# Performance work log

Hardware: AMD Instinct MI355X
Metric: run time of the kernel (lower is better)

## Reference

```python
import jax, jax.numpy as jnp
import numpy as np

EPS = 1e-8
N_NODES, N_EDGES = 10000, 160000
SI, VI = 128, 16          # node scalar / vector channels
ES, EV = 32, 4            # edge scalar / vector channels
SO, VO = 128, 16          # output scalar / vector channels
MSI, MVI = 2 * SI + ES, 2 * VI + EV   # message input dims: 288, 36
H1 = max(MVI, VO)         # layer-1 hidden = 36 (bottleneck=1)
H2 = max(VO, VO)          # layer-2 hidden = 16
SVO = 3                   # scalarization_vectorization_output_dim


def _safe_norm(x, axis):
    return jnp.sqrt(jnp.sum(x * x, axis=axis) + EPS)


def _gcp(s, v, frames, Wdown, Wdf, Wso, bso, Wup, Wg, bg):
    """GCP block on edge-level inputs (node_inputs=False, vector_gate=True).
    s: [E, si], v: [E, vi, 3], frames: [E, 3, 3]."""
    v_pre = jnp.swapaxes(v, -1, -2)                 # [E, 3, vi]
    v_hid = v_pre @ Wdown                           # [E, 3, h]
    v_norm = _safe_norm(v_hid, axis=-2)             # [E, h]
    v_frames = v_pre @ Wdf                          # [E, 3, svo]
    # scalarize: frames @ v_frames -> [E,3,svo], transpose -> [E,svo,3], flatten to 9
    local = jnp.swapaxes(frames @ v_frames, -1, -2).reshape(v.shape[0], 3 * SVO)
    merged = jnp.concatenate([s, v_norm, local], axis=-1)
    s_out = merged @ Wso + bso                      # [E, so]
    v_out = jnp.swapaxes(v_hid @ Wup, -1, -2)       # [E, vo, 3]
    gate = jax.nn.sigmoid(jax.nn.silu(s_out) @ Wg + bg)  # vector gate
    v_out = v_out * gate[..., None]
    return jax.nn.silu(s_out), v_out


def _lin(key, fan_in, fan_out):
    return jax.random.normal(key, (fan_in, fan_out), dtype=jnp.float32) / np.sqrt(fan_in)


def setup_inputs() -> dict:
    key = jax.random.key(0)
    ks = jax.random.split(key, 24)
    M1 = H1 + MSI + 3 * SVO   # 333
    M2 = H2 + SO + 3 * SVO    # 153
    return {
        "node_s": jax.random.normal(ks[0], (N_NODES, SI), dtype=jnp.float32),
        "node_v": jax.random.normal(ks[1], (N_NODES, VI, 3), dtype=jnp.float32),
        "edge_s": jax.random.normal(ks[2], (N_EDGES, ES), dtype=jnp.float32),
        "edge_v": jax.random.normal(ks[3], (N_EDGES, EV, 3), dtype=jnp.float32),
        "frames": jax.random.normal(ks[4], (N_EDGES, 3, 3), dtype=jnp.float32),
        "g1_Wdown": _lin(ks[5], MVI, H1),
        "g1_Wdf": _lin(ks[6], MVI, SVO),
        "g1_Wso": _lin(ks[7], M1, SO),
        "g1_bso": jnp.zeros((SO,), dtype=jnp.float32),
        "g1_Wup": _lin(ks[8], H1, VO),
        "g1_Wg": _lin(ks[9], SO, VO),
        "g1_bg": jnp.zeros((VO,), dtype=jnp.float32),
        "g2_Wdown": _lin(ks[10], VO, H2),
        "g2_Wdf": _lin(ks[11], VO, SVO),
        "g2_Wso": _lin(ks[12], M2, SO),
        "g2_bso": jnp.zeros((SO,), dtype=jnp.float32),
        "g2_Wup": _lin(ks[13], H2, VO),
        "g2_Wg": _lin(ks[14], SO, VO),
        "g2_bg": jnp.zeros((VO,), dtype=jnp.float32),
        "att_W": _lin(ks[15], SO, 1),
        "att_b": jnp.zeros((1,), dtype=jnp.float32),
        "edge_index": jax.random.randint(ks[16], (2, N_EDGES), 0, N_NODES, dtype=jnp.int64),
    }


def reference(node_s, node_v, edge_s, edge_v, frames,
              g1_Wdown, g1_Wdf, g1_Wso, g1_bso, g1_Wup, g1_Wg, g1_bg,
              g2_Wdown, g2_Wdf, g2_Wso, g2_bso, g2_Wup, g2_Wg, g2_bg,
              att_W, att_b, edge_index):
    row, col = edge_index[0], edge_index[1]
    # edge gather: concat source node, edge, dest node features
    ms = jnp.concatenate([node_s[row], edge_s, node_s[col]], axis=-1)   # [E, 288]
    mv = jnp.concatenate([node_v[row], edge_v, node_v[col]], axis=1)    # [E, 36, 3]
    # message_fusion[0]
    s, v = _gcp(ms, mv, frames, g1_Wdown, g1_Wdf, g1_Wso, g1_bso, g1_Wup, g1_Wg, g1_bg)
    # message_fusion[1] with residual
    s2, v2 = _gcp(s, v, frames, g2_Wdown, g2_Wdf, g2_Wso, g2_bso, g2_Wup, g2_Wg, g2_bg)
    s, v = s + s2, v + v2
    # scalar message attention
    attn = jax.nn.sigmoid(s @ att_W + att_b)
    s = s * attn
    # flatten ScalarVector and scatter-sum aggregate to destination nodes
    flat = jnp.concatenate([s, v.reshape(v.shape[0], VO * 3)], axis=-1)  # [E, 176]
    agg = jax.ops.segment_sum(flat, row, num_segments=N_NODES)           # [N, 176]
    return agg
```

## Files before the change

### kernel.cpp

```cpp
#include <hip/hip_runtime.h>
#include <hip/hip_bf16.h>

#define E_TOT 160000
#define NN    10000
#define EPB   32

typedef unsigned short ushortT;
typedef unsigned int   uintT;
typedef __attribute__((ext_vector_type(8))) short short8;
typedef __attribute__((ext_vector_type(4))) float f32x4;

__device__ __forceinline__ float sigmoidf_(float x) { return 1.0f / (1.0f + __expf(-x)); }
__device__ __forceinline__ float siluf_(float x) { return x * sigmoidf_(x); }

__device__ __forceinline__ ushortT f2b(float f) {
    union { float f; uintT u; } x; x.f = f;
    uintT r = x.u + 0x7fffu + ((x.u >> 16) & 1u);
    return (ushortT)(r >> 16);
}
__device__ __forceinline__ float b2f(ushortT h) {
    union { uintT u; float f; } x; x.u = ((uintT)h) << 16; return x.f;
}
__device__ __forceinline__ uintT pk2(float lo, float hi) {
    union { __hip_bfloat162 h; uintT u; } cv;
    cv.h = __float22bfloat162_rn(make_float2(lo, hi));
    return cv.u;
}
__device__ __forceinline__ short8 ldfrag(const float* p) {
    const float4 x = ((const float4*)p)[0];
    const float4 y = ((const float4*)p)[1];
    union { uintT u[4]; short8 s; } r;
    r.u[0] = pk2(x.x, x.y); r.u[1] = pk2(x.z, x.w);
    r.u[2] = pk2(y.x, y.y); r.u[3] = pk2(y.z, y.w);
    return r.s;
}

#define OFF_W1SO 0
#define OFF_W2SO 45056
#define OFF_W1DF 65536
#define OFF_W1G  68608
#define OFF_W1UP 70656
#define OFF_W2DF 71680
#define OFF_W2G  72704
#define OFF_W2UP 74752

#define NOFF_OFF   56320000ULL
#define CUR_OFF    56360016ULL
#define EPOS_OFF   56400032ULL
#define WT_OFF     57040032ULL
#define WS_CSR     57190560ULL
#define NS16_OFF   57190560ULL
#define WS_NS      59750560ULL
#define ES16_OFF   59750560ULL
#define WS_ES      69990560ULL

__global__ __launch_bounds__(256) void prep_kernel(
    const float* __restrict__ W1so, const float* __restrict__ W2so,
    const float* __restrict__ W1d,  const float* __restrict__ W1f,
    const float* __restrict__ W1g,  const float* __restrict__ W1up,
    const float* __restrict__ W2d,  const float* __restrict__ W2f,
    const float* __restrict__ W2g,  const float* __restrict__ W2up,
    ushortT* __restrict__ ws, float* __restrict__ out,
    int* __restrict__ cur, int csr)
{
    int i = blockIdx.x * 256 + threadIdx.x;
    if (csr) {
        if (i < NN) cur[i] = 0;
    } else {
        float4* o4 = (float4*)out;
        #pragma unroll
        for (int k = 0; k < 6; ++k) {
            int z = i + k * 75264;
            if (z < 440000) o4[z] = make_float4(0.f, 0.f, 0.f, 0.f);
        }
    }
    if (i < OFF_W2SO) {
        int n = i / 352, k = i - n * 352;
        ws[i] = (k < 333) ? f2b(W1so[k * 128 + n]) : (ushortT)0;
    } else if (i < OFF_W1DF) {
        int j = i - OFF_W2SO, n = j / 160, k = j - n * 160;
        ws[i] = (k < 153) ? f2b(W2so[k * 128 + n]) : (ushortT)0;
    } else if (i < OFF_W1G) {
        int j = i - OFF_W1DF, n = j / 64, k = j - n * 64;
        float v = 0.f;
        if (k < 36) { if (n < 36) v = W1d[k * 36 + n]; else if (n < 39) v = W1f[k * 3 + (n - 36)]; }
        ws[i] = f2b(v);
    } else if (i < OFF_W1UP) {
        int j = i - OFF_W1G, n = j / 128, k = j - n * 128;
        ws[i] = f2b(W1g[k * 16 + n]);
    } else if (i < OFF_W2DF) {
        int j = i - OFF_W1UP, n = j / 64, k = j - n * 64;
        ws[i] = (k < 36) ? f2b(W1up[k * 16 + n]) : (ushortT)0;
    } else if (i < OFF_W2G) {
        int j = i - OFF_W2DF, n = j / 32, k = j - n * 32;
        float v = 0.f;
        if (k < 16) { if (n < 16) v = W2d[k * 16 + n]; else if (n < 19) v = W2f[k * 3 + (n - 16)]; }
        ws[i] = f2b(v);
    } else if (i < OFF_W2UP) {
        int j = i - OFF_W2G, n = j / 128, k = j - n * 128;
        ws[i] = f2b(W2g[k * 16 + n]);
    } else {
        int j = i - OFF_W2UP, n = j / 32, k = j - n * 32;
        ws[i] = (k < 16) ? f2b(W2up[k * 16 + n]) : (ushortT)0;
    }
}

__device__ __forceinline__ bool idx_is64(const int* pi) {
    return (pi[1] | pi[3] | pi[5] | pi[7] | pi[9] | pi[11] | pi[13] | pi[15]) == 0;
}

__global__ __launch_bounds__(256) void hist_kernel(const void* __restrict__ eidx,
                                                   int* __restrict__ cur,
                                                   const float* __restrict__ node_s,
                                                   const float* __restrict__ edge_s,
                                                   ushortT* __restrict__ ns16,
                                                   ushortT* __restrict__ es16)
{
    int i = blockIdx.x * 256 + threadIdx.x;
    const int* pi = (const int*)eidx;
    const long long* pl = (const long long*)eidx;
    int r = idx_is64(pi) ? (int)pl[i] : pi[i];
    atomicAdd(&cur[r], 1);
    if (ns16) {
        float4 x = ((const float4*)node_s)[i * 2];
        float4 y = ((const float4*)node_s)[i * 2 + 1];
        uint4 st;
        st.x = pk2(x.x, x.y); st.y = pk2(x.z, x.w);
        st.z = pk2(y.x, y.y); st.w = pk2(y.z, y.w);
        ((uint4*)ns16)[i] = st;
    }
    if (es16) {
        #pragma unroll
        for (int k = 0; k < 4; ++k) {
            float4 x = ((const float4*)edge_s)[i * 8 + 2 * k];
            float4 y = ((const float4*)edge_s)[i * 8 + 2 * k + 1];
            uint4 st;
            st.x = pk2(x.x, x.y); st.y = pk2(x.z, x.w);
            st.z = pk2(y.x, y.y); st.w = pk2(y.z, y.w);
            ((uint4*)es16)[i * 4 + k] = st;
        }
    }
}

__global__ __launch_bounds__(256) void scan_kernel(int* __restrict__ cur,
                                                   int* __restrict__ noff)
{
    __shared__ int partial[256];
    const int t = threadIdx.x;
    const int base = t * 40;
    int loc[40];
    int s = 0;
    #pragma unroll
    for (int i = 0; i < 40; ++i) {
        int gi = base + i;
        int v = (gi < NN) ? cur[gi] : 0;
        loc[i] = v; s += v;
    }
    partial[t] = s;
    __syncthreads();
    for (int o = 1; o < 256; o <<= 1) {
        int v = (t >= o) ? partial[t - o] : 0;
        __syncthreads();
        partial[t] += v;
        __syncthreads();
    }
    int run = (t == 0) ? 0 : partial[t - 1];
    #pragma unroll
    for (int i = 0; i < 40; ++i) {
        int gi = base + i;
        if (gi < NN) { noff[gi] = run; run += loc[i]; cur[gi] = 0; }
    }
    if (t == 255) noff[NN] = partial[255];
}

__global__ __launch_bounds__(256) void fill_kernel(const void* __restrict__ eidx,
                                                   const int* __restrict__ noff,
                                                   int* __restrict__ cur,
                                                   int* __restrict__ epos)
{
    int e = blockIdx.x * 256 + threadIdx.x;
    if (e >= E_TOT) return;
    const int* pi = (const int*)eidx;
    const long long* pl = (const long long*)eidx;
    int r = idx_is64(pi) ? (int)pl[e] : pi[e];
    int pos = atomicAdd(&cur[r], 1);
    epos[e] = noff[r] + pos;
}

__global__ __launch_bounds__(256) void node_kernel(const ushortT* __restrict__ fb,
                                                   const int* __restrict__ noff,
                                                   float* __restrict__ out)
{
    const int w = threadIdx.x >> 6, l = threadIdx.x & 63;
    const int n = blockIdx.x * 4 + w;
    if (l >= 44) return;
    const int s = noff[n], eend = noff[n + 1];
    float a0 = 0.f, a1 = 0.f, a2 = 0.f, a3 = 0.f;
    int idx = s;
    for (; idx + 2 <= eend; idx += 2) {
        uint2 p0 = *(const uint2*)(fb + (size_t)idx * 176 + l * 4);
        uint2 p1 = *(const uint2*)(fb + (size_t)(idx + 1) * 176 + l * 4);
        a0 += b2f((ushortT)(p0.x & 0xffff)); a1 += b2f((ushortT)(p0.x >> 16));
        a2 += b2f((ushortT)(p0.y & 0xffff)); a3 += b2f((ushortT)(p0.y >> 16));
        a0 += b2f((ushortT)(p1.x & 0xffff)); a1 += b2f((ushortT)(p1.x >> 16));
        a2 += b2f((ushortT)(p1.y & 0xffff)); a3 += b2f((ushortT)(p1.y >> 16));
    }
    if (idx < eend) {
        uint2 p0 = *(const uint2*)(fb + (size_t)idx * 176 + l * 4);
        a0 += b2f((ushortT)(p0.x & 0xffff)); a1 += b2f((ushortT)(p0.x >> 16));
        a2 += b2f((ushortT)(p0.y & 0xffff)); a3 += b2f((ushortT)(p0.y >> 16));
    }
    ((float4*)(out + (size_t)n * 176))[l] = make_float4(a0, a1, a2, a3);
}

#define MFMA(a, b, c) __builtin_amdgcn_mfma_f32_16x16x32_bf16((a), (b), (c), 0, 0, 0)

__global__ __launch_bounds__(256, 5) void edge_kernel(
    const float* __restrict__ node_s, const float* __restrict__ node_v,
    const float* __restrict__ edge_s, const float* __restrict__ edge_v,
    const float* __restrict__ frames,
    const float* __restrict__ b1so, const float* __restrict__ b1g,
    const float* __restrict__ b2so, const float* __restrict__ b2g,
    const float* __restrict__ attW, const float* __restrict__ attb,
    const ushortT* __restrict__ wsc,
    const void* __restrict__ eidx, float* __restrict__ out,
    ushortT* __restrict__ fb, const int* __restrict__ epos,
    const ushortT* __restrict__ ns16, const ushortT* __restrict__ es16,
    int csr)
{
    const ushortT* W1T   = wsc + OFF_W1SO;
    const ushortT* W2T   = wsc + OFF_W2SO;
    const ushortT* W1dfT = wsc + OFF_W1DF;
    const ushortT* W1gT  = wsc + OFF_W1G;
    const ushortT* W1upT = wsc + OFF_W1UP;
    const ushortT* W2dfT = wsc + OFF_W2DF;
    const ushortT* W2gT  = wsc + OFF_W2G;
    const ushortT* W2upT = wsc + OFF_W2UP;

    __shared__ __align__(16) char smem[31104];
    ushortT* mvA     = (ushortT*)smem;
    ushortT* m2      = (ushortT*)smem;
    ushortT* vhidA   = (ushortT*)(smem + 10752);
    ushortT* s2s     = (ushortT*)(smem + 10752);
    ushortT* normbuf = (ushortT*)(smem + 19456);
    ushortT* v1A     = (ushortT*)(smem + 19456);
    ushortT* vhid2A  = (ushortT*)(smem + 24064);
    float*   vfr2f   = (float*)(smem + 28672);
    float*   fr      = (float*)(smem + 29824);
    float*   attn    = (float*)(smem + 30976);

    const int t  = threadIdx.x;
    const int eg = blockIdx.x * EPB;
    const int w  = t >> 6, lane = t & 63, lq = lane >> 4, ln = lane & 15;
    const int te = t >> 3, tj = t & 7;
    const int p  = w & 1;

    const int* pi = (const int*)eidx;
    const long long* pl = (const long long*)eidx;
    const bool is64 = idx_is64(pi);

    {
        const int nr = is64 ? (int)pl[eg + te] : pi[eg + te];
        const int nc = is64 ? (int)pl[E_TOT + eg + te] : pi[E_TOT + eg + te];
        #pragma unroll
        for (int mi = 0; mi < 2; ++mi) {
            if (mi == 1 && tj != 0) break;
            int m = (mi == 0) ? tj : 8;
            const float* src;
            if (m < 4)       src = node_v + nr * 48 + 12 * m;
            else if (m == 4) src = edge_v + (eg + te) * 12;
            else             src = node_v + nc * 48 + 12 * (m - 5);
            float4 x = ((const float4*)src)[0];
            float4 y = ((const float4*)src)[1];
            float4 z = ((const float4*)src)[2];
            float v[12] = {x.x, x.y, x.z, x.w, y.x, y.y, y.z, y.w, z.x, z.y, z.z, z.w};
            int c0 = 4 * m;
            #pragma unroll
            for (int sp = 0; sp < 3; ++sp) {
                *(uintT*)(mvA + (sp * 32 + te) * 40 + c0)     = pk2(v[sp],     v[3 + sp]);
                *(uintT*)(mvA + (sp * 32 + te) * 40 + c0 + 2) = pk2(v[6 + sp], v[9 + sp]);
            }
        }
        #pragma unroll
        for (int k = 0; k < 2; ++k) {
            int j = tj + k * 8;
            if (j < 9) fr[te * 9 + j] = frames[(eg + te) * 9 + j];
        }
        #pragma unroll
        for (int k = 0; k < 3; ++k) {
            int c = 45 + tj + k * 8;
            if (c < 64) normbuf[te * 72 + c] = 0;
        }
        if (t < 192) {
            int r = t >> 1, cc = 36 + ((t & 1) << 1);
            *(uintT*)(mvA + r * 40 + cc) = 0;
        }
    }
    __syncthreads();

    for (int u = w; u < 18; u += 4) {
        int mt = u / 3, nt = u - mt * 3;
        const ushortT* ap = mvA + (mt * 16 + ln) * 40 + lq * 8;
        const ushortT* bp = W1dfT + (nt * 16 + ln) * 64 + lq * 8;
        f32x4 acc = {0.f, 0.f, 0.f, 0.f};
        acc = MFMA(*(const short8*)ap, *(const short8*)bp, acc);
        short8 a2 = {0, 0, 0, 0, 0, 0, 0, 0};
        if (lq == 0) a2 = *(const short8*)(ap + 32);
        acc = MFMA(a2, *(const short8*)(bp + 32), acc);
        if (nt < 2 || ln < 8) {
            ushortT* op = vhidA + (mt * 16 + lq * 4) * 40 + nt * 16 + ln;
            op[0]   = f2b(acc[0]); op[40]  = f2b(acc[1]);
            op[80]  = f2b(acc[2]); op[120] = f2b(acc[3]);
        }
    }
    __syncthreads();

    {
        #pragma unroll
        for (int k = 0; k < 5; ++k) {
            int h = tj + k * 8;
            if (h < 36) {
                float a0 = b2f(vhidA[te * 40 + h]);
                float a1 = b2f(vhidA[(32 + te) * 40 + h]);
                float a2 = b2f(vhidA[(64 + te) * 40 + h]);
                normbuf[te * 72 + h] = f2b(sqrtf(fmaf(a0, a0, fmaf(a1, a1, fmaf(a2, a2, 1e-8f)))));
            }
        }
        for (int i = t; i < 288; i += 256) {
            int e = i / 9, r = i - e * 9, a = r / 3, b = r - a * 3;
            float x = fr[e * 9 + b * 3 + 0] * b2f(vhidA[e * 40 + 36 + a])
                    + fr[e * 9 + b * 3 + 1] * b2f(vhidA[(32 + e) * 40 + 36 + a])
                    + fr[e * 9 + b * 3 + 2] * b2f(vhidA[(64 + e) * 40 + 36 + a]);
            normbuf[e * 72 + 36 + r] = f2b(x);
        }
    }
    __syncthreads();

    {
        const int klq = lq * 8;
        const int e0 = ln, e1 = 16 + ln;
        int r0, c0, r1, c1;
        if (is64) {
            r0 = (int)pl[eg + e0]; r1 = (int)pl[eg + e1];
            c0 = (int)pl[E_TOT + eg + e0]; c1 = (int)pl[E_TOT + eg + e1];
        } else {
            r0 = pi[eg + e0]; r1 = pi[eg + e1];
            c0 = pi[E_TOT + eg + e0]; c1 = pi[E_TOT + eg + e1];
        }
        r0 *= 128; c0 *= 128; r1 *= 128; c1 *= 128;
        const int eb0 = (eg + e0) * 32, eb1 = (eg + e1) * 32;
        f32x4 acc00 = {0,0,0,0}, acc01 = {0,0,0,0}, acc10 = {0,0,0,0}, acc11 = {0,0,0,0};
        const ushortT* b0p = W1T + (w * 32 + ln) * 352 + klq;
        const ushortT* b1p = W1T + (w * 32 + 16 + ln) * 352 + klq;
        #pragma unroll
        for (int ks = 0; ks < 9; ++ks) {
            short8 a0, a1;
            if (ks < 4) {
                if (ns16) {
                    a0 = *(const short8*)(ns16 + r0 + ks * 32 + klq);
                    a1 = *(const short8*)(ns16 + r1 + ks * 32 + klq);
                } else {
                    a0 = ldfrag(node_s + r0 + ks * 32 + klq);
                    a1 = ldfrag(node_s + r1 + ks * 32 + klq);
                }
            } else if (ks == 4) {
                if (es16) {
                    a0 = *(const short8*)(es16 + eb0 + klq);
                    a1 = *(const short8*)(es16 + eb1 + klq);
                } else {
                    a0 = ldfrag(edge_s + eb0 + klq);
                    a1 = ldfrag(edge_s + eb1 + klq);
                }
            } else {
                if (ns16) {
                    a0 = *(const short8*)(ns16 + c0 + (ks - 5) * 32 + klq);
                    a1 = *(const short8*)(ns16 + c1 + (ks - 5) * 32 + klq);
                } else {
                    a0 = ldfrag(node_s + c0 + (ks - 5) * 32 + klq);
                    a1 = ldfrag(node_s + c1 + (ks - 5) * 32 + klq);
                }
            }
            short8 b0 = *(const short8*)(b0p + ks * 32);
            short8 b1 = *(const short8*)(b1p + ks * 32);
            acc00 = MFMA(a0, b0, acc00); acc01 = MFMA(a0, b1, acc01);
            acc10 = MFMA(a1, b0, acc10); acc11 = MFMA(a1, b1, acc11);
        }
        #pragma unroll
        for (int ks = 9; ks < 11; ++ks) {
            short8 a0 = *(const short8*)(normbuf + e0 * 72 + (ks - 9) * 32 + klq);
            short8 a1 = *(const short8*)(normbuf + e1 * 72 + (ks - 9) * 32 + klq);
            short8 b0 = *(const short8*)(b0p + ks * 32);
            short8 b1 = *(const short8*)(b1p + ks * 32);
            acc00 = MFMA(a0, b0, acc00); acc01 = MFMA(a0, b1, acc01);
            acc10 = MFMA(a1, b0, acc10); acc11 = MFMA(a1, b1, acc11);
        }
        const int n0 = w * 32 + ln, n1 = n0 + 16;
        float bi0 = b1so[n0], bi1 = b1so[n1];
        #pragma unroll
        for (int r = 0; r < 4; ++r) {
            int m0 = lq * 4 + r;
            m2[m0 * 168 + n0]        = f2b(siluf_(acc00[r] + bi0));
            m2[m0 * 168 + n1]        = f2b(siluf_(acc01[r] + bi1));
            m2[(16 + m0) * 168 + n0] = f2b(siluf_(acc10[r] + bi0));
            m2[(16 + m0) * 168 + n1] = f2b(siluf_(acc11[r] + bi1));
        }
    }
    __syncthreads();

    {
        f32x4 gacc = {0,0,0,0};
        {
            const ushortT* ap = m2 + (p * 16 + ln) * 168;
            const ushortT* bp = W1gT + ln * 128;
            #pragma unroll
            for (int ks = 0; ks < 4; ++ks)
                gacc = MFMA(*(const short8*)(ap + ks * 32 + lq * 8),
                            *(const short8*)(bp + ks * 32 + lq * 8), gacc);
        }
        float g1[4];
        {
            float bi = b1g[ln];
            #pragma unroll
            for (int r = 0; r < 4; ++r) g1[r] = sigmoidf_(gacc[r] + bi);
        }
        const ushortT* bpu = W1upT + ln * 64 + lq * 8;
        short8 bu1 = *(const short8*)bpu;
        short8 bu2 = *(const short8*)(bpu + 32);
        #pragma unroll
        for (int c = 0; c < 2; ++c) {
            if (c == 1 && w >= 2) break;
            int mt = w + c * 4;
            const ushortT* ap = vhidA + (mt * 16 + ln) * 40 + lq * 8;
            f32x4 acc = {0,0,0,0};
            acc = MFMA(*(const short8*)ap, bu1, acc);
            short8 a2 = {0, 0, 0, 0, 0, 0, 0, 0};
            if (lq == 0) a2 = *(const short8*)(ap + 32);
            acc = MFMA(a2, bu2, acc);
            #pragma unroll
            for (int r = 0; r < 4; ++r) {
                int row = mt * 16 + lq * 4 + r;
                v1A[row * 24 + ln] = f2b(acc[r] * g1[r]);
            }
        }
        #pragma unroll
        for (int c = 0; c < 2; ++c) {
            if (c == 1 && w >= 2) break;
            int mt = w + c * 4;
            const ushortT* ap = v1A + (mt * 16 + ln) * 24 + lq * 8;
            short8 a = {0, 0, 0, 0, 0, 0, 0, 0};
            if (lq < 2) a = *(const short8*)ap;
            #pragma unroll
            for (int nt = 0; nt < 2; ++nt) {
                const ushortT* bp = W2dfT + (nt * 16 + ln) * 32 + lq * 8;
                f32x4 acc = {0,0,0,0};
                acc = MFMA(a, *(const short8*)bp, acc);
                if (nt == 0) {
                    ushortT* op = vhid2A + (mt * 16 + lq * 4) * 24 + ln;
                    op[0]  = f2b(acc[0]); op[24] = f2b(acc[1]);
                    op[48] = f2b(acc[2]); op[72] = f2b(acc[3]);
                } else if (ln < 3) {
                    float* op = vfr2f + (mt * 16 + lq * 4) * 3 + ln;
                    op[0] = acc[0]; op[3] = acc[1]; op[6] = acc[2]; op[9] = acc[3];
                }
            }
        }
    }
    __syncthreads();

    {
        #pragma unroll
        for (int k = 0; k < 2; ++k) {
            int i = t + k * 256, e = i >> 4, h = i & 15;
            float a0 = b2f(vhid2A[e * 24 + h]);
            float a1 = b2f(vhid2A[(32 + e) * 24 + h]);
            float a2 = b2f(vhid2A[(64 + e) * 24 + h]);
            m2[e * 168 + 128 + h] = f2b(sqrtf(fmaf(a0, a0, fmaf(a1, a1, fmaf(a2, a2, 1e-8f)))));
        }
        for (int i = t; i < 288; i += 256) {
            int e = i / 9, r = i - e * 9, a = r / 3, b = r - a * 3;
            float x = fr[e * 9 + b * 3 + 0] * vfr2f[e * 3 + a]
                    + fr[e * 9 + b * 3 + 1] * vfr2f[(32 + e) * 3 + a]
                    + fr[e * 9 + b * 3 + 2] * vfr2f[(64 + e) * 3 + a];
            m2[e * 168 + 144 + r] = f2b(x);
        }
        if (tj) m2[te * 168 + 152 + tj] = 0;
    }
    __syncthreads();

    {
        f32x4 acc00 = {0,0,0,0}, acc01 = {0,0,0,0}, acc10 = {0,0,0,0}, acc11 = {0,0,0,0};
        const ushortT* a0p = m2 + ln * 168 + lq * 8;
        const ushortT* a1p = m2 + (16 + ln) * 168 + lq * 8;
        const ushortT* b0p = W2T + (w * 32 + ln) * 160 + lq * 8;
        const ushortT* b1p = W2T + (w * 32 + 16 + ln) * 160 + lq * 8;
        #pragma unroll
        for (int ks = 0; ks < 5; ++ks) {
            short8 a0 = *(const short8*)(a0p + ks * 32);
            short8 a1 = *(const short8*)(a1p + ks * 32);
            short8 b0 = *(const short8*)(b0p + ks * 32);
            short8 b1 = *(const short8*)(b1p + ks * 32);
            acc00 = MFMA(a0, b0, acc00); acc01 = MFMA(a0, b1, acc01);
            acc10 = MFMA(a1, b0, acc10); acc11 = MFMA(a1, b1, acc11);
        }
        const int n0 = w * 32 + ln, n1 = n0 + 16;
        float bi0 = b2so[n0], bi1 = b2so[n1];
        #pragma unroll
        for (int r = 0; r < 4; ++r) {
            int m0 = lq * 4 + r;
            s2s[m0 * 136 + n0]        = f2b(siluf_(acc00[r] + bi0));
            s2s[m0 * 136 + n1]        = f2b(siluf_(acc01[r] + bi1));
            s2s[(16 + m0) * 136 + n0] = f2b(siluf_(acc10[r] + bi0));
            s2s[(16 + m0) * 136 + n1] = f2b(siluf_(acc11[r] + bi1));
        }
    }
    __syncthreads();

    {
        f32x4 gacc = {0,0,0,0};
        {
            const ushortT* ap = s2s + (p * 16 + ln) * 136;
            const ushortT* bp = W2gT + ln * 128;
            #pragma unroll
            for (int ks = 0; ks < 4; ++ks)
                gacc = MFMA(*(const short8*)(ap + ks * 32 + lq * 8),
                            *(const short8*)(bp + ks * 32 + lq * 8), gacc);
        }
        float g2[4];
        {
            float bi = b2g[ln];
            #pragma unroll
            for (int r = 0; r < 4; ++r) g2[r] = sigmoidf_(gacc[r] + bi);
        }
        const ushortT* bpu = W2upT + ln * 32 + lq * 8;
        short8 bu = *(const short8*)bpu;
        #pragma unroll
        for (int c = 0; c < 2; ++c) {
            if (c == 1 && w >= 2) break;
            int mt = w + c * 4;
            const ushortT* ap = vhid2A + (mt * 16 + ln) * 24 + lq * 8;
            short8 a = {0, 0, 0, 0, 0, 0, 0, 0};
            if (lq < 2) a = *(const short8*)ap;
            f32x4 acc = {0,0,0,0};
            acc = MFMA(a, bu, acc);
            #pragma unroll
            for (int r = 0; r < 4; ++r) {
                int row = mt * 16 + lq * 4 + r;
                float vfin = b2f(v1A[row * 24 + ln]) + acc[r] * g2[r];
                v1A[row * 24 + ln] = f2b(vfin);
            }
        }
        {
            float sum = 0.f;
            int c0 = tj * 16;
            #pragma unroll
            for (int c = c0; c < c0 + 16; ++c)
                sum = fmaf(b2f(m2[te * 168 + c]) + b2f(s2s[te * 136 + c]), attW[c], sum);
            sum += __shfl_xor(sum, 4);
            sum += __shfl_xor(sum, 2);
            sum += __shfl_xor(sum, 1);
            if (tj == 0) attn[te] = sigmoidf_(sum + attb[0]);
        }
    }
    __syncthreads();

    {
        const float at = attn[te];
        if (csr) {
            const int pos = epos[eg + te];
            ushortT* fbe = fb + (size_t)pos * 176;
            #pragma unroll
            for (int k = 0; k < 11; ++k) {
                int j = 2 * tj + 16 * k;
                float v0, v1;
                if (j < 128) {
                    v0 = (b2f(m2[te * 168 + j])     + b2f(s2s[te * 136 + j]))     * at;
                    v1 = (b2f(m2[te * 168 + j + 1]) + b2f(s2s[te * 136 + j + 1])) * at;
                } else {
                    int r = j - 128;
                    int o0 = r / 3,        sp0 = r - o0 * 3;
                    int o1 = (r + 1) / 3,  sp1 = (r + 1) - o1 * 3;
                    v0 = b2f(v1A[(sp0 * 32 + te) * 24 + o0]);
                    v1 = b2f(v1A[(sp1 * 32 + te) * 24 + o1]);
                }
                *(uintT*)(fbe + j) = pk2(v0, v1);
            }
        } else {
            const int nr = is64 ? (int)pl[eg + te] : pi[eg + te];
            const int orow = nr * 176;
            #pragma unroll
            for (int k = 0; k < 22; ++k) {
                int j = tj + k * 8;
                float val;
                if (j < 128) {
                    val = (b2f(m2[te * 168 + j]) + b2f(s2s[te * 136 + j])) * at;
                } else {
                    int r = j - 128, o = r / 3, sp = r - o * 3;
                    val = b2f(v1A[(sp * 32 + te) * 24 + o]);
                }
                atomicAdd(&out[orow + j], val);
            }
        }
    }
}

extern "C" void kernel_launch(void* const* d_in, const int* in_sizes, int n_in,
                              void* d_out, int out_size, void* d_ws, size_t ws_size,
                              hipStream_t stream) {
    const float* node_s = (const float*)d_in[0];
    const float* node_v = (const float*)d_in[1];
    const float* edge_s = (const float*)d_in[2];
    const float* edge_v = (const float*)d_in[3];
    const float* frames = (const float*)d_in[4];
    const float* W1d  = (const float*)d_in[5];
    const float* W1f  = (const float*)d_in[6];
    const float* W1so = (const float*)d_in[7];
    const float* b1so = (const float*)d_in[8];
    const float* W1up = (const float*)d_in[9];
    const float* W1g  = (const float*)d_in[10];
    const float* b1g  = (const float*)d_in[11];
    const float* W2d  = (const float*)d_in[12];
    const float* W2f  = (const float*)d_in[13];
    const float* W2so = (const float*)d_in[14];
    const float* b2so = (const float*)d_in[15];
    const float* W2up = (const float*)d_in[16];
    const float* W2g  = (const float*)d_in[17];
    const float* b2g  = (const float*)d_in[18];
    const float* attW = (const float*)d_in[19];
    const float* attb = (const float*)d_in[20];
    const void*  eidx = d_in[21];

    float* out = (float*)d_out;
    char* ws = (char*)d_ws;

    int mode = 0;
    if (ws_size >= WS_ES)       mode = 3;
    else if (ws_size >= WS_NS)  mode = 2;
    else if (ws_size >= WS_CSR) mode = 1;
    const int csr = (mode >= 1);

    ushortT* wt    = csr ? (ushortT*)(ws + WT_OFF)  : (ushortT*)ws;
    ushortT* fbuf  = csr ? (ushortT*)ws             : nullptr;
    int*     noff  = csr ? (int*)(ws + NOFF_OFF)    : nullptr;
    int*     cur   = csr ? (int*)(ws + CUR_OFF)     : nullptr;
    int*     epos  = csr ? (int*)(ws + EPOS_OFF)    : nullptr;
    ushortT* ns16  = (mode >= 2) ? (ushortT*)(ws + NS16_OFF) : nullptr;
    ushortT* es16  = (mode >= 3) ? (ushortT*)(ws + ES16_OFF) : nullptr;

    prep_kernel<<<294, 256, 0, stream>>>(W1so, W2so, W1d, W1f, W1g, W1up,
                                         W2d, W2f, W2g, W2up, wt, out, cur, csr);

    if (csr) {
        hist_kernel<<<625, 256, 0, stream>>>(eidx, cur, node_s, edge_s, ns16, es16);
        scan_kernel<<<1, 256, 0, stream>>>(cur, noff);
        fill_kernel<<<625, 256, 0, stream>>>(eidx, noff, cur, epos);
    }

    edge_kernel<<<E_TOT / EPB, 256, 0, stream>>>(
        node_s, node_v, edge_s, edge_v, frames,
        b1so, b1g, b2so, b2g, attW, attb,
        (const ushortT*)wt, eidx, out, fbuf, epos, ns16, es16, csr);

    if (csr) {
        node_kernel<<<2500, 256, 0, stream>>>((const ushortT*)fbuf, noff, out);
    }
}
```

Measured before the change: 333.2 us.

## Fuse CSR setup kernels and compute edge slot positions inside edge kernel

Weight conversion is merged into the histogram kernel, and the separate fill kernel is removed. Each edge now claims its CSR slot with an atomic inside the edge kernel just before it writes its message, so the epos array and one full pass over the edges go away. The counter reset becomes a memset, and the scan stages counts in shared memory. Fewer launches and less global traffic are the goal. The cost is atomic contention added to the edge kernel's epilogue, and the slot order within each node now depends on block scheduling, so summation order is nondeterministic.

```diff
diff --git a/kernel.cpp b/kernel.cpp
--- a/kernel.cpp
+++ b/kernel.cpp
@@ -43,10 +43,10 @@
 #define OFF_W2DF 71680
 #define OFF_W2G  72704
 #define OFF_W2UP 74752
+#define WT_USH   75264
 
 #define NOFF_OFF   56320000ULL
 #define CUR_OFF    56360016ULL
-#define EPOS_OFF   56400032ULL
 #define WT_OFF     57040032ULL
 #define WS_CSR     57190560ULL
 #define NS16_OFF   57190560ULL
@@ -54,26 +54,19 @@
 #define ES16_OFF   59750560ULL
 #define WS_ES      69990560ULL
 
-__global__ __launch_bounds__(256) void prep_kernel(
+__device__ __forceinline__ bool idx_is64(const int* pi) {
+    return (pi[1] | pi[3] | pi[5] | pi[7] | pi[9] | pi[11] | pi[13] | pi[15]) == 0;
+}
+
+__device__ __forceinline__ void weight_prep(
+    int i,
     const float* __restrict__ W1so, const float* __restrict__ W2so,
     const float* __restrict__ W1d,  const float* __restrict__ W1f,
     const float* __restrict__ W1g,  const float* __restrict__ W1up,
     const float* __restrict__ W2d,  const float* __restrict__ W2f,
     const float* __restrict__ W2g,  const float* __restrict__ W2up,
-    ushortT* __restrict__ ws, float* __restrict__ out,
-    int* __restrict__ cur, int csr)
+    ushortT* __restrict__ ws)
 {
-    int i = blockIdx.x * 256 + threadIdx.x;
-    if (csr) {
-        if (i < NN) cur[i] = 0;
-    } else {
-        float4* o4 = (float4*)out;
-        #pragma unroll
-        for (int k = 0; k < 6; ++k) {
-            int z = i + k * 75264;
-            if (z < 440000) o4[z] = make_float4(0.f, 0.f, 0.f, 0.f);
-        }
-    }
     if (i < OFF_W2SO) {
         int n = i / 352, k = i - n * 352;
         ws[i] = (k < 333) ? f2b(W1so[k * 128 + n]) : (ushortT)0;
@@ -99,29 +92,31 @@
     } else if (i < OFF_W2UP) {
         int j = i - OFF_W2G, n = j / 128, k = j - n * 128;
         ws[i] = f2b(W2g[k * 16 + n]);
-    } else {
+    } else if (i < WT_USH) {
         int j = i - OFF_W2UP, n = j / 32, k = j - n * 32;
         ws[i] = (k < 16) ? f2b(W2up[k * 16 + n]) : (ushortT)0;
     }
 }
 
-__device__ __forceinline__ bool idx_is64(const int* pi) {
-    return (pi[1] | pi[3] | pi[5] | pi[7] | pi[9] | pi[11] | pi[13] | pi[15]) == 0;
-}
-
-__global__ __launch_bounds__(256) void hist_kernel(const void* __restrict__ eidx,
-                                                   int* __restrict__ cur,
-                                                   const float* __restrict__ node_s,
-                                                   const float* __restrict__ edge_s,
-                                                   ushortT* __restrict__ ns16,
-                                                   ushortT* __restrict__ es16)
+__global__ __launch_bounds__(256) void setup_kernel(
+    const float* __restrict__ W1so, const float* __restrict__ W2so,
+    const float* __restrict__ W1d,  const float* __restrict__ W1f,
+    const float* __restrict__ W1g,  const float* __restrict__ W1up,
+    const float* __restrict__ W2d,  const float* __restrict__ W2f,
+    const float* __restrict__ W2g,  const float* __restrict__ W2up,
+    ushortT* __restrict__ ws,
+    const void* __restrict__ eidx, int* __restrict__ cur,
+    const float* __restrict__ node_s, const float* __restrict__ edge_s,
+    ushortT* __restrict__ ns16, ushortT* __restrict__ es16)
 {
     int i = blockIdx.x * 256 + threadIdx.x;
-    const int* pi = (const int*)eidx;
-    const long long* pl = (const long long*)eidx;
-    int r = idx_is64(pi) ? (int)pl[i] : pi[i];
-    atomicAdd(&cur[r], 1);
-    if (ns16) {
+    {
+        const int* pi = (const int*)eidx;
+        const long long* pl = (const long long*)eidx;
+        int r = idx_is64(pi) ? (int)pl[i] : pi[i];
+        atomicAdd(&cur[r], 1);
+    }
+    if (ns16 && i < 160000) {
         float4 x = ((const float4*)node_s)[i * 2];
         float4 y = ((const float4*)node_s)[i * 2 + 1];
         uint4 st;
@@ -140,22 +135,40 @@
             ((uint4*)es16)[i * 4 + k] = st;
         }
     }
+    weight_prep(i, W1so, W2so, W1d, W1f, W1g, W1up, W2d, W2f, W2g, W2up, ws);
+}
+
+__global__ __launch_bounds__(256) void prep_kernel(
+    const float* __restrict__ W1so, const float* __restrict__ W2so,
+    const float* __restrict__ W1d,  const float* __restrict__ W1f,
+    const float* __restrict__ W1g,  const float* __restrict__ W1up,
+    const float* __restrict__ W2d,  const float* __restrict__ W2f,
+    const float* __restrict__ W2g,  const float* __restrict__ W2up,
+    ushortT* __restrict__ ws, float* __restrict__ out)
+{
+    int i = blockIdx.x * 256 + threadIdx.x;
+    float4* o4 = (float4*)out;
+    #pragma unroll
+    for (int k = 0; k < 6; ++k) {
+        int z = i + k * 75264;
+        if (z < 440000) o4[z] = make_float4(0.f, 0.f, 0.f, 0.f);
+    }
+    weight_prep(i, W1so, W2so, W1d, W1f, W1g, W1up, W2d, W2f, W2g, W2up, ws);
 }
 
 __global__ __launch_bounds__(256) void scan_kernel(int* __restrict__ cur,
                                                    int* __restrict__ noff)
 {
+    __shared__ int buf[10000];
     __shared__ int partial[256];
     const int t = threadIdx.x;
+    for (int i = t; i < NN; i += 256) buf[i] = cur[i];
+    for (int i = t; i < NN; i += 256) cur[i] = 0;
+    __syncthreads();
     const int base = t * 40;
-    int loc[40];
     int s = 0;
     #pragma unroll
-    for (int i = 0; i < 40; ++i) {
-        int gi = base + i;
-        int v = (gi < NN) ? cur[gi] : 0;
-        loc[i] = v; s += v;
-    }
+    for (int i = 0; i < 40; ++i) s += (base + i < NN) ? buf[base + i] : 0;
     partial[t] = s;
     __syncthreads();
     for (int o = 1; o < 256; o <<= 1) {
@@ -168,23 +181,9 @@
     #pragma unroll
     for (int i = 0; i < 40; ++i) {
         int gi = base + i;
-        if (gi < NN) { noff[gi] = run; run += loc[i]; cur[gi] = 0; }
+        if (gi < NN) { int v = buf[gi]; noff[gi] = run; run += v; }
     }
     if (t == 255) noff[NN] = partial[255];
-}
-
-__global__ __launch_bounds__(256) void fill_kernel(const void* __restrict__ eidx,
-                                                   const int* __restrict__ noff,
-                                                   int* __restrict__ cur,
-                                                   int* __restrict__ epos)
-{
-    int e = blockIdx.x * 256 + threadIdx.x;
-    if (e >= E_TOT) return;
-    const int* pi = (const int*)eidx;
-    const long long* pl = (const long long*)eidx;
-    int r = idx_is64(pi) ? (int)pl[e] : pi[e];
-    int pos = atomicAdd(&cur[r], 1);
-    epos[e] = noff[r] + pos;
 }
 
 __global__ __launch_bounds__(256) void node_kernel(const ushortT* __restrict__ fb,
@@ -224,7 +223,7 @@
     const float* __restrict__ attW, const float* __restrict__ attb,
     const ushortT* __restrict__ wsc,
     const void* __restrict__ eidx, float* __restrict__ out,
-    ushortT* __restrict__ fb, const int* __restrict__ epos,
+    ushortT* __restrict__ fb, int* __restrict__ cur, const int* __restrict__ noff,
     const ushortT* __restrict__ ns16, const ushortT* __restrict__ es16,
     int csr)
 {
@@ -237,7 +236,7 @@
     const ushortT* W2gT  = wsc + OFF_W2G;
     const ushortT* W2upT = wsc + OFF_W2UP;
 
-    __shared__ __align__(16) char smem[31104];
+    __shared__ __align__(16) char smem[31232];
     ushortT* mvA     = (ushortT*)smem;
     ushortT* m2      = (ushortT*)smem;
     ushortT* vhidA   = (ushortT*)(smem + 10752);
@@ -248,6 +247,7 @@
     float*   vfr2f   = (float*)(smem + 28672);
     float*   fr      = (float*)(smem + 29824);
     float*   attn    = (float*)(smem + 30976);
+    int*     eposb   = (int*)(smem + 31104);
 
     const int t  = threadIdx.x;
     const int eg = blockIdx.x * EPB;
@@ -560,13 +560,18 @@
             sum += __shfl_xor(sum, 1);
             if (tj == 0) attn[te] = sigmoidf_(sum + attb[0]);
         }
+        if (csr && tj == 0) {
+            int nr = is64 ? (int)pl[eg + te] : pi[eg + te];
+            int pos = atomicAdd(&cur[nr], 1);
+            eposb[te] = noff[nr] + pos;
+        }
     }
     __syncthreads();
 
     {
         const float at = attn[te];
         if (csr) {
-            const int pos = epos[eg + te];
+            const int pos = eposb[te];
             ushortT* fbe = fb + (size_t)pos * 176;
             #pragma unroll
             for (int k = 0; k < 11; ++k) {
@@ -642,23 +647,24 @@
     ushortT* fbuf  = csr ? (ushortT*)ws             : nullptr;
     int*     noff  = csr ? (int*)(ws + NOFF_OFF)    : nullptr;
     int*     cur   = csr ? (int*)(ws + CUR_OFF)     : nullptr;
-    int*     epos  = csr ? (int*)(ws + EPOS_OFF)    : nullptr;
     ushortT* ns16  = (mode >= 2) ? (ushortT*)(ws + NS16_OFF) : nullptr;
     ushortT* es16  = (mode >= 3) ? (ushortT*)(ws + ES16_OFF) : nullptr;
 
-    prep_kernel<<<294, 256, 0, stream>>>(W1so, W2so, W1d, W1f, W1g, W1up,
-                                         W2d, W2f, W2g, W2up, wt, out, cur, csr);
-
     if (csr) {
-        hist_kernel<<<625, 256, 0, stream>>>(eidx, cur, node_s, edge_s, ns16, es16);
+        hipMemsetAsync(cur, 0, NN * sizeof(int), stream);
+        setup_kernel<<<625, 256, 0, stream>>>(
+            W1so, W2so, W1d, W1f, W1g, W1up, W2d, W2f, W2g, W2up,
+            wt, eidx, cur, node_s, edge_s, ns16, es16);
         scan_kernel<<<1, 256, 0, stream>>>(cur, noff);
-        fill_kernel<<<625, 256, 0, stream>>>(eidx, noff, cur, epos);
+    } else {
+        prep_kernel<<<294, 256, 0, stream>>>(W1so, W2so, W1d, W1f, W1g, W1up,
+                                             W2d, W2f, W2g, W2up, wt, out);
     }
 
     edge_kernel<<<E_TOT / EPB, 256, 0, stream>>>(
         node_s, node_v, edge_s, edge_v, frames,
         b1so, b1g, b2so, b2g, attW, attb,
-        (const ushortT*)wt, eidx, out, fbuf, epos, ns16, es16, csr);
+        (const ushortT*)wt, eidx, out, fbuf, cur, noff, ns16, es16, csr);
 
     if (csr) {
         node_kernel<<<2500, 256, 0, stream>>>((const ushortT*)fbuf, noff, out);
```

Result: faster. 312.2 us (-6.3%).
